# Kernel tuning notes

Measured on AMD Instinct MI355X. Metric: run time of the kernel, lower is better.

Reference implementation:

```python
import jax, jax.numpy as jnp
import numpy as np

B, S, D = 2, 2048, 1024
H = 16
HD = D // H  # head_dim = 64
NEG = -1e30  # finite stand-in for -inf; masked entries are zeroed after softmax so math matches


def setup_inputs() -> dict:
    key = jax.random.key(0)
    ks = jax.random.split(key, 10)
    q = jax.random.normal(ks[0], (B, S, D), dtype=jnp.float32)
    k = jax.random.normal(ks[1], (B, S, D), dtype=jnp.float32)
    v = jax.random.normal(ks[2], (B, S, D), dtype=jnp.float32)
    mask = jax.random.randint(ks[3], (B, S), 0, 2).astype(bool)
    s = 1.0 / np.sqrt(D)
    Wq = jax.random.uniform(ks[4], (D, D), jnp.float32, -s, s)
    bq = jax.random.uniform(ks[5], (D,), jnp.float32, -s, s)
    Wk = jax.random.uniform(ks[6], (D, D), jnp.float32, -s, s)
    bk = jax.random.uniform(ks[7], (D,), jnp.float32, -s, s)
    Wv = jax.random.uniform(ks[8], (D, D), jnp.float32, -s, s)
    bv = jax.random.uniform(ks[9], (D,), jnp.float32, -s, s)
    return {"q": q, "k": k, "v": v, "mask": mask,
            "Wq": Wq, "bq": bq, "Wk": Wk, "bk": bk, "Wv": Wv, "bv": bv}


def _split_heads(x):
    # [B,S,D] -> [H,B,S,HD]  (matches permute(2,0,1,3) in torch)
    return x.reshape(B, S, H, HD).transpose(2, 0, 1, 3)


def reference(q, k, v, mask, Wq, bq, Wk, bk, Wv, bv):
    mq = _split_heads(q @ Wq.T + bq)
    mk = _split_heads(k @ Wk.T + bk)
    mv = _split_heads(v @ Wv.T + bv)
    # scores: [H,B,Sq,Sk]
    scores = jnp.einsum('hbqd,hbkd->hbqk', mq, mk) / jnp.sqrt(jnp.float32(HD))
    pair_mask = (mask[:, :, None] & mask[:, None, :])[None]  # [1,B,S,S]
    scores = jnp.where(pair_mask, scores, NEG)
    attn = jax.nn.softmax(scores, axis=-1)
    attn = jnp.where(pair_mask, attn, 0.0)
    out = jnp.einsum('hbqk,hbkd->hbqd', attn, mv)
    # [H,B,S,HD] -> [B,S,D]
    return out.transpose(1, 2, 0, 3).reshape(B, S, H * HD)
```

## Files before the change

kernel.cpp:

```cpp
#include <hip/hip_runtime.h>
#include <math.h>

#define B_ 2
#define S_ 2048
#define D_ 1024
#define H_ 16
#define HD_ 64

#define LOG2E 1.44269504088896f
#define LN2   0.69314718055994531f

typedef __bf16 bf16_t;
typedef bf16_t bf16x8 __attribute__((ext_vector_type(8)));
typedef bf16_t bf16x4v __attribute__((ext_vector_type(4)));
typedef float f32x4 __attribute__((ext_vector_type(4)));

#if defined(__has_builtin)
#  if __has_builtin(__builtin_amdgcn_exp2f)
#    define EXP2(x) __builtin_amdgcn_exp2f(x)
#  else
#    define EXP2(x) __expf((x) * LN2)
#  endif
#else
#  define EXP2(x) __expf((x) * LN2)
#endif

#define GLOBAL_LOAD_LDS16(gp, lp)                                              \
    __builtin_amdgcn_global_load_lds(                                          \
        (const __attribute__((address_space(1))) void*)(gp),                   \
        (__attribute__((address_space(3))) void*)(lp), 16, 0, 0)

__global__ __launch_bounds__(256) void cvt_kernel(
    const float* __restrict__ q, const float* __restrict__ k,
    const float* __restrict__ v, const float* __restrict__ wq,
    const float* __restrict__ wk, const float* __restrict__ wv,
    const int* __restrict__ msk,
    bf16_t* __restrict__ qb, bf16_t* __restrict__ kb, bf16_t* __restrict__ vb,
    bf16_t* __restrict__ wqb, bf16_t* __restrict__ wkb, bf16_t* __restrict__ wvb,
    float* __restrict__ kbias)
{
    const int bid = blockIdx.x;
    const float* src;
    bf16_t* dst;
    int x;

    if (bid < 12288) {
        int y = bid >> 12;
        x = bid & 4095;
        src = (y == 0) ? q : (y == 1) ? k : v;
        dst = (y == 0) ? qb : (y == 1) ? kb : vb;
    } else if (bid < 15360) {
        int y = (bid - 12288) >> 10;
        x = (bid - 12288) & 1023;
        src = (y == 0) ? wq : (y == 1) ? wk : wv;
        dst = (y == 0) ? wqb : (y == 1) ? wkb : wvb;
    } else {
        size_t idx = ((size_t)(bid - 15360) * 256 + threadIdx.x) * 4;
        int4 mi = *(const int4*)(msk + idx);
        const float vb_ = -8.0f * LOG2E;
        float4 o4;
        o4.x = mi.x ? vb_ : -1e30f;
        o4.y = mi.y ? vb_ : -1e30f;
        o4.z = mi.z ? vb_ : -1e30f;
        o4.w = mi.w ? vb_ : -1e30f;
        *(float4*)(kbias + idx) = o4;
        return;
    }

    size_t idx = ((size_t)x * 256 + threadIdx.x) * 4;
    float4 f = *(const float4*)(src + idx);
    bf16x4v o;
    o[0] = (bf16_t)f.x; o[1] = (bf16_t)f.y;
    o[2] = (bf16_t)f.z; o[3] = (bf16_t)f.w;
    *(bf16x4v*)(dst + idx) = o;
}

__global__ __launch_bounds__(256) void proj_mfma(
    const bf16_t* __restrict__ X0, const bf16_t* __restrict__ X1,
    const bf16_t* __restrict__ X2, const bf16_t* __restrict__ W0,
    const bf16_t* __restrict__ W1, const bf16_t* __restrict__ W2,
    const float* __restrict__ b0, const float* __restrict__ b1,
    const float* __restrict__ b2, bf16_t* __restrict__ o0,
    bf16_t* __restrict__ o1, bf16_t* __restrict__ o2)
{
    __shared__ __align__(16) bf16_t As[128 * 32];
    __shared__ __align__(16) bf16_t Bs[128 * 32];

    const int z = blockIdx.z;
    const bf16_t* X = (z == 0) ? X0 : (z == 1) ? X1 : X2;
    const bf16_t* W = (z == 0) ? W0 : (z == 1) ? W1 : W2;
    const float* bias = (z == 0) ? b0 : (z == 1) ? b1 : b2;
    bf16_t* out = (z == 0) ? o0 : (z == 1) ? o1 : o2;

    const bf16_t* Amat = (z == 2) ? X : W;
    const bf16_t* Bmat = (z == 2) ? W : X;
    const int arow0 = (z == 2) ? blockIdx.x * 128 : blockIdx.y * 128;
    const int brow0 = (z == 2) ? blockIdx.y * 128 : blockIdx.x * 128;

    const int tid  = threadIdx.x;
    const int w    = tid >> 6;
    const int lane = tid & 63;
    const int L    = lane & 15;
    const int quad = lane >> 4;
    const int wr   = (w >> 1) * 64;
    const int wc   = (w & 1) * 64;

    const int lr = lane >> 2;
    const int lc = (lane & 3) * 8;

    f32x4 acc[4][4];
    #pragma unroll
    for (int i = 0; i < 4; ++i)
        #pragma unroll
        for (int j = 0; j < 4; ++j) {
            acc[i][j][0] = 0.f; acc[i][j][1] = 0.f;
            acc[i][j][2] = 0.f; acc[i][j][3] = 0.f;
        }

    for (int k0 = 0; k0 < D_; k0 += 32) {
        __syncthreads();
        #pragma unroll
        for (int i = 0; i < 2; ++i) {
            const int rA = i * 64 + w * 16;
            GLOBAL_LOAD_LDS16(Amat + (size_t)(arow0 + rA + lr) * D_ + k0 + lc,
                              &As[rA * 32]);
            GLOBAL_LOAD_LDS16(Bmat + (size_t)(brow0 + rA + lr) * D_ + k0 + lc,
                              &Bs[rA * 32]);
        }
        __syncthreads();

        bf16x8 aF[4], bF[4];
        #pragma unroll
        for (int t = 0; t < 4; ++t) {
            aF[t] = *(const bf16x8*)&As[(wr + t * 16 + L) * 32 + quad * 8];
            bF[t] = *(const bf16x8*)&Bs[(wc + t * 16 + L) * 32 + quad * 8];
        }
        #pragma unroll
        for (int mt = 0; mt < 4; ++mt)
            #pragma unroll
            for (int nt = 0; nt < 4; ++nt)
                acc[mt][nt] = __builtin_amdgcn_mfma_f32_16x16x32_bf16(
                    aF[mt], bF[nt], acc[mt][nt], 0, 0, 0);
    }

    if (z == 2) {
        #pragma unroll
        for (int nt = 0; nt < 4; ++nt) {
            const int j  = brow0 + wc + nt * 16 + L;
            const float bval = bias[j];
            const int h  = j >> 6;
            const int hd = j & 63;
            #pragma unroll
            for (int mt = 0; mt < 4; ++mt) {
                const int n = arow0 + wr + mt * 16 + quad * 4;
                const int b = n >> 11;
                const int s = n & (S_ - 1);
                bf16x4v r4;
                #pragma unroll
                for (int r = 0; r < 4; ++r)
                    r4[r] = (bf16_t)(acc[mt][nt][r] + bval);
                *(bf16x4v*)(out + (((size_t)b * H_ + h) * HD_ + hd) * S_ + s) = r4;
            }
        }
    } else {
        const float oscale = (z == 0) ? 0.125f * LOG2E : 1.0f;
        #pragma unroll
        for (int mt = 0; mt < 4; ++mt) {
            const int j4 = arow0 + wr + mt * 16 + quad * 4;
            const int h  = j4 >> 6;
            const int hd = j4 & 63;
            const f32x4 b4 = *(const f32x4*)(bias + j4);
            #pragma unroll
            for (int nt = 0; nt < 4; ++nt) {
                const int n = brow0 + wc + nt * 16 + L;
                const int b = n >> 11;
                const int s = n & (S_ - 1);
                bf16x4v r4;
                #pragma unroll
                for (int r = 0; r < 4; ++r)
                    r4[r] = (bf16_t)((acc[mt][nt][r] + b4[r]) * oscale);
                *(bf16x4v*)(out + ((((size_t)b * H_ + h) * S_ + s) * HD_) + hd) = r4;
            }
        }
    }
}

__global__ __launch_bounds__(256) void attn_kernel(
    const bf16_t* __restrict__ Q, const bf16_t* __restrict__ K,
    const bf16_t* __restrict__ Vt, const float* __restrict__ kbias,
    const int* __restrict__ mask, float* __restrict__ out)
{
    constexpr int LD = 72;
    __shared__ bf16_t Ks[64 * LD];
    __shared__ bf16_t Vs[64 * LD];
    __shared__ bf16_t Pt[4][32 * LD];

    const int tid  = threadIdx.x;
    const int w    = tid >> 6;
    const int lane = tid & 63;
    const int L    = lane & 15;
    const int quad = lane >> 4;
    const int h    = blockIdx.y;
    const int b    = blockIdx.z;
    const int bh   = b * H_ + h;
    const int q0   = blockIdx.x * 128;

    const bf16_t* kbase = K  + (size_t)bh * S_ * HD_;
    const bf16_t* vbase = Vt + (size_t)bh * HD_ * S_;
    const float*  bbase = kbias + b * S_;
    const int*    mrow  = mask + b * S_;

    const int sr  = tid >> 3;
    const int sc2 = (tid & 7) * 8;

    bf16x8 aQ[2][2];
    #pragma unroll
    for (int qb = 0; qb < 2; ++qb) {
        const bf16_t* qp = Q + ((size_t)bh * S_ + q0 + w * 32 + qb * 16 + L) * HD_;
        aQ[qb][0] = *(const bf16x8*)(qp + quad * 8);
        aQ[qb][1] = *(const bf16x8*)(qp + 32 + quad * 8);
    }

    f32x4 o[2][4];
    #pragma unroll
    for (int qb = 0; qb < 2; ++qb)
        #pragma unroll
        for (int f = 0; f < 4; ++f) {
            o[qb][f][0]=0.f; o[qb][f][1]=0.f; o[qb][f][2]=0.f; o[qb][f][3]=0.f;
        }
    float l_[2] = {0.f, 0.f};

    bf16x8 kr0, kr1, vr0, vr1;
    f32x4  bias_n[4];
    {
        kr0 = *(const bf16x8*)(kbase + (size_t)sr * HD_ + sc2);
        kr1 = *(const bf16x8*)(kbase + (size_t)(sr + 32) * HD_ + sc2);
        vr0 = *(const bf16x8*)(vbase + (size_t)sr * S_ + sc2);
        vr1 = *(const bf16x8*)(vbase + (size_t)(sr + 32) * S_ + sc2);
        #pragma unroll
        for (int f = 0; f < 4; ++f)
            bias_n[f] = *(const f32x4*)(bbase + f * 16 + quad * 4);
    }

    for (int kt = 0; kt < S_; kt += 64) {
        __syncthreads();
        *(bf16x8*)&Ks[sr * LD + sc2]        = kr0;
        *(bf16x8*)&Ks[(sr + 32) * LD + sc2] = kr1;
        *(bf16x8*)&Vs[sr * LD + sc2]        = vr0;
        *(bf16x8*)&Vs[(sr + 32) * LD + sc2] = vr1;
        f32x4 bias_c[4];
        #pragma unroll
        for (int f = 0; f < 4; ++f) bias_c[f] = bias_n[f];
        __syncthreads();

        if (kt + 64 < S_) {
            const int kn = kt + 64;
            kr0 = *(const bf16x8*)(kbase + (size_t)(kn + sr) * HD_ + sc2);
            kr1 = *(const bf16x8*)(kbase + (size_t)(kn + sr + 32) * HD_ + sc2);
            vr0 = *(const bf16x8*)(vbase + (size_t)sr * S_ + kn + sc2);
            vr1 = *(const bf16x8*)(vbase + (size_t)(sr + 32) * S_ + kn + sc2);
            #pragma unroll
            for (int f = 0; f < 4; ++f)
                bias_n[f] = *(const f32x4*)(bbase + kn + f * 16 + quad * 4);
        }

        bf16x8 aK[4][2];
        #pragma unroll
        for (int f = 0; f < 4; ++f) {
            aK[f][0] = *(const bf16x8*)&Ks[(f * 16 + L) * LD + quad * 8];
            aK[f][1] = *(const bf16x8*)&Ks[(f * 16 + L) * LD + 32 + quad * 8];
        }

        bf16_t* pw = &Pt[w][0];
        #pragma unroll
        for (int qb = 0; qb < 2; ++qb) {
            #pragma unroll
            for (int f = 0; f < 4; ++f) {
                f32x4 z = bias_c[f];
                z = __builtin_amdgcn_mfma_f32_16x16x32_bf16(aK[f][0], aQ[qb][0], z, 0, 0, 0);
                z = __builtin_amdgcn_mfma_f32_16x16x32_bf16(aK[f][1], aQ[qb][1], z, 0, 0, 0);
                float e0 = EXP2(z[0]);
                float e1 = EXP2(z[1]);
                float e2 = EXP2(z[2]);
                float e3 = EXP2(z[3]);
                l_[qb] += (e0 + e1) + (e2 + e3);
                bf16x4v p4;
                p4[0] = (bf16_t)e0; p4[1] = (bf16_t)e1;
                p4[2] = (bf16_t)e2; p4[3] = (bf16_t)e3;
                *(bf16x4v*)&pw[(qb * 16 + L) * LD + f * 16 + quad * 4] = p4;
            }
        }

        bf16x8 aP[2][2];
        #pragma unroll
        for (int qb = 0; qb < 2; ++qb) {
            aP[qb][0] = *(const bf16x8*)&pw[(qb * 16 + L) * LD + quad * 8];
            aP[qb][1] = *(const bf16x8*)&pw[(qb * 16 + L) * LD + 32 + quad * 8];
        }

        #pragma unroll
        for (int f = 0; f < 4; ++f) {
            bf16x8 bV0 = *(const bf16x8*)&Vs[(f * 16 + L) * LD + quad * 8];
            bf16x8 bV1 = *(const bf16x8*)&Vs[(f * 16 + L) * LD + 32 + quad * 8];
            #pragma unroll
            for (int qb = 0; qb < 2; ++qb) {
                o[qb][f] = __builtin_amdgcn_mfma_f32_16x16x32_bf16(aP[qb][0], bV0, o[qb][f], 0, 0, 0);
                o[qb][f] = __builtin_amdgcn_mfma_f32_16x16x32_bf16(aP[qb][1], bV1, o[qb][f], 0, 0, 0);
            }
        }
    }

    #pragma unroll
    for (int qb = 0; qb < 2; ++qb) {
        float t = l_[qb];
        t += __shfl_xor(t, 16);
        t += __shfl_xor(t, 32);
        int qv = mrow[q0 + w * 32 + qb * 16 + L];
        l_[qb] = (qv && t > 0.f) ? (1.0f / t) : 0.0f;
    }

    #pragma unroll
    for (int qb = 0; qb < 2; ++qb) {
        float inv[4];
        #pragma unroll
        for (int r = 0; r < 4; ++r)
            inv[r] = __shfl(l_[qb], quad * 4 + r);
        float* obase = out + ((size_t)b * S_ + q0 + w * 32 + qb * 16 + quad * 4) * D_ + h * HD_;
        #pragma unroll
        for (int f = 0; f < 4; ++f)
            #pragma unroll
            for (int r = 0; r < 4; ++r)
                obase[r * D_ + f * 16 + L] = o[qb][f][r] * inv[r];
    }
}

extern "C" void kernel_launch(void* const* d_in, const int* in_sizes, int n_in,
                              void* d_out, int out_size, void* d_ws, size_t ws_size,
                              hipStream_t stream)
{
    const float* q    = (const float*)d_in[0];
    const float* k    = (const float*)d_in[1];
    const float* v    = (const float*)d_in[2];
    const int*   mask = (const int*)d_in[3];
    const float* Wq   = (const float*)d_in[4];
    const float* bq   = (const float*)d_in[5];
    const float* Wk   = (const float*)d_in[6];
    const float* bk   = (const float*)d_in[7];
    const float* Wv   = (const float*)d_in[8];
    const float* bv   = (const float*)d_in[9];
    float* out = (float*)d_out;

    const size_t PE = (size_t)B_ * S_ * D_;
    const size_t WE = (size_t)D_ * D_;

    bf16_t* qb    = (bf16_t*)d_ws;
    bf16_t* kb    = qb + PE;
    bf16_t* vb    = kb + PE;
    bf16_t* wqb   = vb + PE;
    bf16_t* wkb   = wqb + WE;
    bf16_t* wvb   = wkb + WE;
    bf16_t* mq    = wvb + WE;
    bf16_t* mk    = mq + PE;
    bf16_t* vt    = mk + PE;
    float*  kbias = (float*)(vt + PE);

    cvt_kernel<<<dim3(15364), 256, 0, stream>>>(q, k, v, Wq, Wk, Wv, mask,
                                                qb, kb, vb, wqb, wkb, wvb, kbias);

    dim3 pgrid(4096 / 128, 1024 / 128, 3);
    proj_mfma<<<pgrid, 256, 0, stream>>>(qb, kb, vb, wqb, wkb, wvb,
                                         bq, bk, bv, mq, mk, vt);

    dim3 agrid(S_ / 128, H_, B_);
    attn_kernel<<<agrid, 256, 0, stream>>>(mq, mk, vt, kbias, mask, out);
}
```

Baseline: 212.5 us.

## Split key tile across warps, keep P in registers, reduce outputs in LDS

Each block now handles 64 queries instead of 128, so the grid is twice as large. Each warp takes a 16-key slice of every 64-key tile instead of 32 queries. The softmax probabilities go straight from the QK MFMA accumulators into zero-padded MFMA operands for PV, which removes the shared-memory round trip for P. Per-warp partial outputs and row sums are then combined through an LDS reduction before the normalized store. In exchange, half of every PV MFMA is padding, more MFMAs are spent per query-key pair, K/V global reads double, and the serialized cross-warp reduction adds extra barriers.

```diff
diff --git a/kernel.cpp b/kernel.cpp
--- a/kernel.cpp
+++ b/kernel.cpp
@@ -185,15 +185,17 @@
     }
 }
 
-__global__ __launch_bounds__(256) void attn_kernel(
+__global__ __launch_bounds__(256, 3) void attn_kernel(
     const bf16_t* __restrict__ Q, const bf16_t* __restrict__ K,
     const bf16_t* __restrict__ Vt, const float* __restrict__ kbias,
     const int* __restrict__ mask, float* __restrict__ out)
 {
     constexpr int LD = 72;
+    constexpr int OD = 68;
     __shared__ bf16_t Ks[64 * LD];
     __shared__ bf16_t Vs[64 * LD];
-    __shared__ bf16_t Pt[4][32 * LD];
+    __shared__ float  obuf[64 * OD];
+    __shared__ float  lbuf[4][64];
 
     const int tid  = threadIdx.x;
     const int w    = tid >> 6;
@@ -203,7 +205,7 @@
     const int h    = blockIdx.y;
     const int b    = blockIdx.z;
     const int bh   = b * H_ + h;
-    const int q0   = blockIdx.x * 128;
+    const int q0   = blockIdx.x * 64;
 
     const bf16_t* kbase = K  + (size_t)bh * S_ * HD_;
     const bf16_t* vbase = Vt + (size_t)bh * HD_ * S_;
@@ -213,33 +215,31 @@
     const int sr  = tid >> 3;
     const int sc2 = (tid & 7) * 8;
 
-    bf16x8 aQ[2][2];
-    #pragma unroll
-    for (int qb = 0; qb < 2; ++qb) {
-        const bf16_t* qp = Q + ((size_t)bh * S_ + q0 + w * 32 + qb * 16 + L) * HD_;
-        aQ[qb][0] = *(const bf16x8*)(qp + quad * 8);
-        aQ[qb][1] = *(const bf16x8*)(qp + 32 + quad * 8);
-    }
-
-    f32x4 o[2][4];
-    #pragma unroll
-    for (int qb = 0; qb < 2; ++qb)
-        #pragma unroll
-        for (int f = 0; f < 4; ++f) {
-            o[qb][f][0]=0.f; o[qb][f][1]=0.f; o[qb][f][2]=0.f; o[qb][f][3]=0.f;
-        }
-    float l_[2] = {0.f, 0.f};
+    bf16x8 aQ[4][2];
+    #pragma unroll
+    for (int qg = 0; qg < 4; ++qg) {
+        const bf16_t* qp = Q + ((size_t)bh * S_ + q0 + qg * 16 + L) * HD_;
+        aQ[qg][0] = *(const bf16x8*)(qp + quad * 8);
+        aQ[qg][1] = *(const bf16x8*)(qp + 32 + quad * 8);
+    }
+
+    f32x4 o[4][4];
+    #pragma unroll
+    for (int qg = 0; qg < 4; ++qg)
+        #pragma unroll
+        for (int dg = 0; dg < 4; ++dg) {
+            o[qg][dg][0]=0.f; o[qg][dg][1]=0.f; o[qg][dg][2]=0.f; o[qg][dg][3]=0.f;
+        }
+    float l_[4] = {0.f, 0.f, 0.f, 0.f};
 
     bf16x8 kr0, kr1, vr0, vr1;
-    f32x4  bias_n[4];
+    f32x4  bias_n;
     {
         kr0 = *(const bf16x8*)(kbase + (size_t)sr * HD_ + sc2);
         kr1 = *(const bf16x8*)(kbase + (size_t)(sr + 32) * HD_ + sc2);
         vr0 = *(const bf16x8*)(vbase + (size_t)sr * S_ + sc2);
         vr1 = *(const bf16x8*)(vbase + (size_t)(sr + 32) * S_ + sc2);
-        #pragma unroll
-        for (int f = 0; f < 4; ++f)
-            bias_n[f] = *(const f32x4*)(bbase + f * 16 + quad * 4);
+        bias_n = *(const f32x4*)(bbase + w * 16 + quad * 4);
     }
 
     for (int kt = 0; kt < S_; kt += 64) {
@@ -248,9 +248,7 @@
         *(bf16x8*)&Ks[(sr + 32) * LD + sc2] = kr1;
         *(bf16x8*)&Vs[sr * LD + sc2]        = vr0;
         *(bf16x8*)&Vs[(sr + 32) * LD + sc2] = vr1;
-        f32x4 bias_c[4];
-        #pragma unroll
-        for (int f = 0; f < 4; ++f) bias_c[f] = bias_n[f];
+        f32x4 bias_c = bias_n;
         __syncthreads();
 
         if (kt + 64 < S_) {
@@ -259,78 +257,93 @@
             kr1 = *(const bf16x8*)(kbase + (size_t)(kn + sr + 32) * HD_ + sc2);
             vr0 = *(const bf16x8*)(vbase + (size_t)sr * S_ + kn + sc2);
             vr1 = *(const bf16x8*)(vbase + (size_t)(sr + 32) * S_ + kn + sc2);
-            #pragma unroll
-            for (int f = 0; f < 4; ++f)
-                bias_n[f] = *(const f32x4*)(bbase + kn + f * 16 + quad * 4);
-        }
-
-        bf16x8 aK[4][2];
-        #pragma unroll
-        for (int f = 0; f < 4; ++f) {
-            aK[f][0] = *(const bf16x8*)&Ks[(f * 16 + L) * LD + quad * 8];
-            aK[f][1] = *(const bf16x8*)&Ks[(f * 16 + L) * LD + 32 + quad * 8];
-        }
-
-        bf16_t* pw = &Pt[w][0];
-        #pragma unroll
-        for (int qb = 0; qb < 2; ++qb) {
-            #pragma unroll
-            for (int f = 0; f < 4; ++f) {
-                f32x4 z = bias_c[f];
-                z = __builtin_amdgcn_mfma_f32_16x16x32_bf16(aK[f][0], aQ[qb][0], z, 0, 0, 0);
-                z = __builtin_amdgcn_mfma_f32_16x16x32_bf16(aK[f][1], aQ[qb][1], z, 0, 0, 0);
-                float e0 = EXP2(z[0]);
-                float e1 = EXP2(z[1]);
-                float e2 = EXP2(z[2]);
-                float e3 = EXP2(z[3]);
-                l_[qb] += (e0 + e1) + (e2 + e3);
-                bf16x4v p4;
-                p4[0] = (bf16_t)e0; p4[1] = (bf16_t)e1;
-                p4[2] = (bf16_t)e2; p4[3] = (bf16_t)e3;
-                *(bf16x4v*)&pw[(qb * 16 + L) * LD + f * 16 + quad * 4] = p4;
-            }
-        }
-
-        bf16x8 aP[2][2];
-        #pragma unroll
-        for (int qb = 0; qb < 2; ++qb) {
-            aP[qb][0] = *(const bf16x8*)&pw[(qb * 16 + L) * LD + quad * 8];
-            aP[qb][1] = *(const bf16x8*)&pw[(qb * 16 + L) * LD + 32 + quad * 8];
-        }
-
-        #pragma unroll
-        for (int f = 0; f < 4; ++f) {
-            bf16x8 bV0 = *(const bf16x8*)&Vs[(f * 16 + L) * LD + quad * 8];
-            bf16x8 bV1 = *(const bf16x8*)&Vs[(f * 16 + L) * LD + 32 + quad * 8];
-            #pragma unroll
-            for (int qb = 0; qb < 2; ++qb) {
-                o[qb][f] = __builtin_amdgcn_mfma_f32_16x16x32_bf16(aP[qb][0], bV0, o[qb][f], 0, 0, 0);
-                o[qb][f] = __builtin_amdgcn_mfma_f32_16x16x32_bf16(aP[qb][1], bV1, o[qb][f], 0, 0, 0);
-            }
-        }
-    }
-
-    #pragma unroll
-    for (int qb = 0; qb < 2; ++qb) {
-        float t = l_[qb];
+            bias_n = *(const f32x4*)(bbase + kn + w * 16 + quad * 4);
+        }
+
+        bf16x8 aK0 = *(const bf16x8*)&Ks[(w * 16 + L) * LD + quad * 8];
+        bf16x8 aK1 = *(const bf16x8*)&Ks[(w * 16 + L) * LD + 32 + quad * 8];
+
+        bf16x8 pA[4];
+        #pragma unroll
+        for (int qg = 0; qg < 4; ++qg) {
+            f32x4 z;
+            z[0] = bias_c[0]; z[1] = bias_c[1];
+            z[2] = bias_c[2]; z[3] = bias_c[3];
+            z = __builtin_amdgcn_mfma_f32_16x16x32_bf16(aK0, aQ[qg][0], z, 0, 0, 0);
+            z = __builtin_amdgcn_mfma_f32_16x16x32_bf16(aK1, aQ[qg][1], z, 0, 0, 0);
+            float e0 = EXP2(z[0]);
+            float e1 = EXP2(z[1]);
+            float e2 = EXP2(z[2]);
+            float e3 = EXP2(z[3]);
+            l_[qg] += (e0 + e1) + (e2 + e3);
+            bf16x8 p8;
+            p8[0] = (bf16_t)e0; p8[1] = (bf16_t)e1;
+            p8[2] = (bf16_t)e2; p8[3] = (bf16_t)e3;
+            p8[4] = (bf16_t)0.f; p8[5] = (bf16_t)0.f;
+            p8[6] = (bf16_t)0.f; p8[7] = (bf16_t)0.f;
+            pA[qg] = p8;
+        }
+
+        #pragma unroll
+        for (int dg = 0; dg < 4; ++dg) {
+            bf16x4v v4 = *(const bf16x4v*)&Vs[(dg * 16 + L) * LD + w * 16 + quad * 4];
+            bf16x8 bv8;
+            bv8[0] = v4[0]; bv8[1] = v4[1]; bv8[2] = v4[2]; bv8[3] = v4[3];
+            bv8[4] = (bf16_t)0.f; bv8[5] = (bf16_t)0.f;
+            bv8[6] = (bf16_t)0.f; bv8[7] = (bf16_t)0.f;
+            #pragma unroll
+            for (int qg = 0; qg < 4; ++qg)
+                o[qg][dg] = __builtin_amdgcn_mfma_f32_16x16x32_bf16(
+                    pA[qg], bv8, o[qg][dg], 0, 0, 0);
+        }
+    }
+
+    #pragma unroll
+    for (int qg = 0; qg < 4; ++qg) {
+        float t = l_[qg];
         t += __shfl_xor(t, 16);
         t += __shfl_xor(t, 32);
-        int qv = mrow[q0 + w * 32 + qb * 16 + L];
-        l_[qb] = (qv && t > 0.f) ? (1.0f / t) : 0.0f;
-    }
-
-    #pragma unroll
-    for (int qb = 0; qb < 2; ++qb) {
-        float inv[4];
-        #pragma unroll
-        for (int r = 0; r < 4; ++r)
-            inv[r] = __shfl(l_[qb], quad * 4 + r);
-        float* obase = out + ((size_t)b * S_ + q0 + w * 32 + qb * 16 + quad * 4) * D_ + h * HD_;
-        #pragma unroll
-        for (int f = 0; f < 4; ++f)
-            #pragma unroll
-            for (int r = 0; r < 4; ++r)
-                obase[r * D_ + f * 16 + L] = o[qb][f][r] * inv[r];
+        if (lane < 16) lbuf[w][qg * 16 + L] = t;
+    }
+
+    if (w == 0) {
+        #pragma unroll
+        for (int qg = 0; qg < 4; ++qg)
+            #pragma unroll
+            for (int dg = 0; dg < 4; ++dg)
+                *(f32x4*)&obuf[(dg * 16 + L) * OD + qg * 16 + quad * 4] = o[qg][dg];
+    }
+    __syncthreads();
+    #pragma unroll
+    for (int ww = 1; ww < 4; ++ww) {
+        if (w == ww) {
+            #pragma unroll
+            for (int qg = 0; qg < 4; ++qg)
+                #pragma unroll
+                for (int dg = 0; dg < 4; ++dg) {
+                    float* dst = &obuf[(dg * 16 + L) * OD + qg * 16 + quad * 4];
+                    f32x4 t = *(const f32x4*)dst;
+                    t[0] += o[qg][dg][0]; t[1] += o[qg][dg][1];
+                    t[2] += o[qg][dg][2]; t[3] += o[qg][dg][3];
+                    *(f32x4*)dst = t;
+                }
+        }
+        __syncthreads();
+    }
+
+    const int q = tid >> 2;
+    const int c = (tid & 3) * 16;
+    float lt = lbuf[0][q] + lbuf[1][q] + lbuf[2][q] + lbuf[3][q];
+    int qv = mrow[q0 + q];
+    float inv = (qv && lt > 0.f) ? (1.0f / lt) : 0.0f;
+    float* op = out + ((size_t)b * S_ + q0 + q) * D_ + h * HD_ + c;
+    #pragma unroll
+    for (int g = 0; g < 4; ++g) {
+        f32x4 rr;
+        #pragma unroll
+        for (int j = 0; j < 4; ++j)
+            rr[j] = obuf[(c + g * 4 + j) * OD + q] * inv;
+        *(f32x4*)(op + g * 4) = rr;
     }
 }
 
@@ -371,6 +384,6 @@
     proj_mfma<<<pgrid, 256, 0, stream>>>(qb, kb, vb, wqb, wkb, wvb,
                                          bq, bk, bv, mq, mk, vt);
 
-    dim3 agrid(S_ / 128, H_, B_);
+    dim3 agrid(S_ / 64, H_, B_);
     attn_kernel<<<agrid, 256, 0, stream>>>(mq, mk, vt, kbias, mask, out);
 }
```

Measured after the change: 221.2 us. +4.1%, slower.
